# Optimization experiments

Measured on AMD Instinct MI355X. Metric: run time of the kernel, lower is better.

## Reference

```python
import jax, jax.numpy as jnp
import numpy as np

B, P, NP, D, DS, M, K = 2, 4000, 4096, 64, 64, 512, 8
NX, NY = 432, 496
HW = NY * NX


def _per_batch(points, pillars, pillars_scale, idx, W):
    # points: [NP, D], pillars: [P, D], pillars_scale: [P, DS], idx: [P] in [0, HW)
    # --- get_score: top-k point attention per pillar ---
    score = jax.nn.softmax(points @ pillars.T, axis=0)                # [NP, P], softmax over points
    top_idx = jax.lax.top_k(jax.lax.stop_gradient(score).T, K)[1]     # [P, K]
    pts_pos = points[top_idx]                                         # [P, K, D]
    agg = jax.nn.softmax(jnp.einsum('pd,pkd->pk', pillars, pts_pos), axis=1)
    pos_point = jnp.einsum('pk,pkd->pd', jax.lax.stop_gradient(agg), pts_pos)  # [P, D]
    # --- memory unit: top-k memory-item attention per pillar ---
    att = jax.nn.softmax(pillars @ W.T, axis=1)                       # [P, M]
    midx = jax.lax.top_k(jax.lax.stop_gradient(att), K)[1]            # [P, K]
    mem_pos = W[midx]                                                 # [P, K, D]
    magg = jax.nn.softmax(jnp.einsum('pd,pkd->pk', pillars, mem_pos), axis=1)
    pos_mem = jnp.einsum('pk,pkd->pd', magg, mem_pos)                 # [P, D]
    # --- scatter into dense BEV grids ---
    sp_point = jnp.zeros((2 * D, HW), pillars.dtype).at[:, idx].set(
        jnp.concatenate([pillars, pos_point], axis=1).T)
    sp = jnp.zeros((2 * D, HW), pillars.dtype).at[:, idx].set(
        jnp.concatenate([jax.lax.stop_gradient(pillars), pos_mem], axis=1).T)
    sp_scale = jnp.zeros((DS, HW), pillars_scale.dtype).at[:, idx].set(pillars_scale.T)
    return sp, sp_point, sp_scale, pos_point, pos_mem


def setup_inputs() -> dict:
    key = jax.random.key(0)
    k1, k2, k3, k4, k5 = jax.random.split(key, 5)
    return {
        'pillar_features': jax.random.normal(k1, (B, P, D), jnp.float32),
        'pillar_scale_features': jax.random.normal(k2, (B, P, DS), jnp.float32),
        'point_features': jax.random.normal(k3, (B, NP, D), jnp.float32),
        'memory_weight': jax.random.normal(k4, (M, D), jnp.float32),
        'indices': jax.random.randint(k5, (B, P), 0, HW, jnp.int32),
    }


def reference(pillar_features, pillar_scale_features, point_features, memory_weight, indices):
    sp, sp_point, sp_scale, pos_point, pos_mem = jax.vmap(
        _per_batch, in_axes=(0, 0, 0, 0, None))(
        point_features, pillar_features, pillar_scale_features, indices, memory_weight)
    spatial_features = sp.reshape(B, 2 * D, NY, NX)
    spatial_features_point = sp_point.reshape(B, 2 * D, NY, NX)
    spatial_scale_features = sp_scale.reshape(B, DS, NY, NX)
    point_positive_features = pos_point.reshape(B * P, D)
    memory_positive_features = pos_mem.reshape(B * P, D)
    return (spatial_features, spatial_features_point, spatial_scale_features,
            point_positive_features, memory_positive_features)
```

## Files before the change

kernel.cpp:

```cpp
#include <hip/hip_runtime.h>

#define B_     2
#define P_TOT  4000
#define NP_TOT 4096
#define D_     64
#define M_     512
#define HW_TOT 214272
#define J4     53568

#define O0 0UL
#define O1 54853632UL
#define O2 109707264UL
#define O3 137134080UL
#define O4 137646080UL

typedef __attribute__((ext_vector_type(8))) short bb8;
typedef __attribute__((ext_vector_type(4))) float f32x4;

__device__ __forceinline__ void insert8(float sc, int n, float s[8], int ix[8]) {
  float cs = sc; int ci = n;
#pragma unroll
  for (int i = 0; i < 8; ++i) {
    bool gt = cs > s[i];
    float ts = s[i]; int ti = ix[i];
    s[i]  = gt ? cs : ts;  ix[i] = gt ? ci : ti;
    cs    = gt ? ts : cs;  ci    = gt ? ti : ci;
  }
}

__device__ __forceinline__ void split_bf16(float x, short& h, short& l) {
  unsigned fb = __float_as_uint(x);
  unsigned hb = fb & 0xFFFF0000u;
  float lof = x - __uint_as_float(hb);
  h = (short)(hb >> 16);
  l = (short)(__float_as_uint(lof) >> 16);
}

__global__ __launch_bounds__(256) void prep(
    const float* __restrict__ points, short* __restrict__ hi, short* __restrict__ lo,
    const int* __restrict__ indices, int* __restrict__ owner,
    const float* __restrict__ W, short* __restrict__ whi, short* __restrict__ wlo)
{
  if (blockIdx.x < 512) {
    int t = blockIdx.x * 256 + threadIdx.x;
    float4 v = ((const float4*)points)[t];
    float x[4] = {v.x, v.y, v.z, v.w};
    short h[4], l[4];
#pragma unroll
    for (int j = 0; j < 4; ++j) split_bf16(x[j], h[j], l[j]);
    ((short4*)hi)[t] = make_short4(h[0], h[1], h[2], h[3]);
    ((short4*)lo)[t] = make_short4(l[0], l[1], l[2], l[3]);
  } else if (blockIdx.x < 544) {
    int t = (blockIdx.x - 512) * 256 + threadIdx.x;
    if (t >= B_ * P_TOT) return;
    int b = (t >= P_TOT) ? 1 : 0;
    int p = t - b * P_TOT;
    atomicMax(&owner[b * HW_TOT + indices[t]], p);
  } else {
    int t = (blockIdx.x - 544) * 256 + threadIdx.x;
    float4 v = ((const float4*)W)[t];
    float x[4] = {v.x, v.y, v.z, v.w};
    short h[4], l[4];
#pragma unroll
    for (int j = 0; j < 4; ++j) split_bf16(x[j], h[j], l[j]);
    ((short4*)whi)[t] = make_short4(h[0], h[1], h[2], h[3]);
    ((short4*)wlo)[t] = make_short4(l[0], l[1], l[2], l[3]);
  }
}

__global__ __launch_bounds__(256) void topk_mfma(
    const float* __restrict__ pillars,
    const short* __restrict__ phi, const short* __restrict__ plo,
    const short* __restrict__ whi, const short* __restrict__ wlo,
    float* __restrict__ ws_pts_sc, int* __restrict__ ws_pts_ix,
    float* __restrict__ ws_mem_sc, int* __restrict__ ws_mem_ix)
{
  const int tid = threadIdx.x;
  const int pt = blockIdx.x, chy = blockIdx.y, b = blockIdx.z;
  const bool is_mem = chy >= 8;
  const int ch = is_mem ? (chy - 8) : chy;
  const int lane = tid & 63, wv = tid >> 6;
  const int sub = lane & 15, quad = lane >> 4;

  int prow = pt * 64 + wv * 16 + sub;
  if (prow >= P_TOT) prow = P_TOT - 1;
  const float* ap = pillars + ((size_t)(b * P_TOT) + prow) * D_;
  bb8 Ah0, Ah1, Al0, Al1;
  {
    const float4* a4 = (const float4*)(ap + quad * 8);
    const float4* b4 = (const float4*)(ap + 32 + quad * 8);
    float4 t0 = a4[0], t1 = a4[1], t2 = b4[0], t3 = b4[1];
    float av[16] = {t0.x, t0.y, t0.z, t0.w, t1.x, t1.y, t1.z, t1.w,
                    t2.x, t2.y, t2.z, t2.w, t3.x, t3.y, t3.z, t3.w};
#pragma unroll
    for (int j = 0; j < 8; ++j) {
      short h, l;
      split_bf16(av[j], h, l);     Ah0[j] = h; Al0[j] = l;
      split_bf16(av[8 + j], h, l); Ah1[j] = h; Al1[j] = l;
    }
  }

  float sv[4][8]; int iv[4][8];
#pragma unroll
  for (int r = 0; r < 4; ++r)
#pragma unroll
    for (int k = 0; k < 8; ++k) { sv[r][k] = -1e30f; iv[r][k] = 0; }

  const short* bh;
  const short* bl;
  int iters, ngb;
  if (is_mem) {
    bh = whi + (size_t)(ch * 64) * D_;
    bl = wlo + (size_t)(ch * 64) * D_;
    iters = 4;  ngb = ch * 64;
  } else {
    const size_t bofs = ((size_t)(b * NP_TOT) + ch * 512) * D_;
    bh = phi + bofs;  bl = plo + bofs;
    iters = 32; ngb = ch * 512;
  }

#pragma unroll 2
  for (int it = 0; it < iters; ++it) {
    const int nr = it * 16 + sub;
    const short* rh = bh + nr * D_;
    const short* rl = bl + nr * D_;
    bb8 Bh0 = *(const bb8*)(rh + quad * 8);
    bb8 Bh1 = *(const bb8*)(rh + 32 + quad * 8);
    bb8 Bl0 = *(const bb8*)(rl + quad * 8);
    bb8 Bl1 = *(const bb8*)(rl + 32 + quad * 8);
    f32x4 acc = {0.f, 0.f, 0.f, 0.f};
    if (is_mem) {
      acc = __builtin_amdgcn_mfma_f32_16x16x32_bf16(Al0, Bl0, acc, 0, 0, 0);
      acc = __builtin_amdgcn_mfma_f32_16x16x32_bf16(Al1, Bl1, acc, 0, 0, 0);
    }
    acc = __builtin_amdgcn_mfma_f32_16x16x32_bf16(Al0, Bh0, acc, 0, 0, 0);
    acc = __builtin_amdgcn_mfma_f32_16x16x32_bf16(Al1, Bh1, acc, 0, 0, 0);
    acc = __builtin_amdgcn_mfma_f32_16x16x32_bf16(Ah0, Bl0, acc, 0, 0, 0);
    acc = __builtin_amdgcn_mfma_f32_16x16x32_bf16(Ah1, Bl1, acc, 0, 0, 0);
    acc = __builtin_amdgcn_mfma_f32_16x16x32_bf16(Ah0, Bh0, acc, 0, 0, 0);
    acc = __builtin_amdgcn_mfma_f32_16x16x32_bf16(Ah1, Bh1, acc, 0, 0, 0);
    const int ng = ngb + nr;
#pragma unroll
    for (int r = 0; r < 4; ++r) {
      float sc = acc[r];
      if (sc > sv[r][7]) insert8(sc, ng, sv[r], iv[r]);
    }
  }

  float* osc = is_mem ? ws_mem_sc : ws_pts_sc;
  int*   oix = is_mem ? ws_mem_ix : ws_pts_ix;

  const int pbase = pt * 64 + wv * 16 + quad * 4;
#pragma unroll
  for (int r = 0; r < 4; ++r) {
    const int pg = pbase + r;
    float out_s = 0.f; int out_i = 0;
#pragma unroll
    for (int k = 0; k < 8; ++k) {
      unsigned fb = __float_as_uint(sv[r][0]);
      unsigned mk = (fb & 0x80000000u) ? ~fb : (fb | 0x80000000u);
      unsigned key = (mk & 0xFFFFFFF0u) | (unsigned)sub;
#pragma unroll
      for (int off = 1; off < 16; off <<= 1) {
        unsigned ok = (unsigned)__shfl_xor((int)key, off);
        key = key > ok ? key : ok;
      }
      const int wsub = (int)(key & 15u);
      const int wlane = (lane & 48) | wsub;
      float wsc = __shfl(sv[r][0], wlane);
      int   wix = __shfl(iv[r][0], wlane);
      if (sub == wsub) {
#pragma unroll
        for (int i2 = 0; i2 < 7; ++i2) { sv[r][i2] = sv[r][i2 + 1]; iv[r][i2] = iv[r][i2 + 1]; }
        sv[r][7] = -1e30f;
      }
      if (sub == k) { out_s = wsc; out_i = wix; }
    }
    if (sub < 8 && pg < P_TOT) {
      const size_t base = ((size_t)(b * P_TOT) + pg) * 64 + ch * 8 + sub;
      osc[base] = out_s; oix[base] = out_i;
    }
  }
}

__global__ __launch_bounds__(256) void finalize2(
    const float* __restrict__ points, const float* __restrict__ W,
    const float* __restrict__ ws_sc_p, const int* __restrict__ ws_ix_p,
    const float* __restrict__ ws_sc_m, const int* __restrict__ ws_ix_m,
    float* __restrict__ out_p, float* __restrict__ out_m)
{
  const int tid = threadIdx.x;
  const int lane = tid & 63, wv = tid >> 6;
  const int gp = blockIdx.x * 4 + wv;
  const int b = (gp >= P_TOT) ? 1 : 0;
  const size_t cb = (size_t)gp * 64;
  const bool mem = (blockIdx.y == 1);

  const float* ws_sc = mem ? ws_sc_m : ws_sc_p;
  const int*   ws_ix = mem ? ws_ix_m : ws_ix_p;
  const float* sb    = mem ? W : (points + (size_t)b * (NP_TOT * D_));
  float*       outp  = mem ? out_m : out_p;

  float ss = ws_sc[cb + lane];
  const int myix = ws_ix[cb + lane];

  float wsc[8]; int wix[8];
#pragma unroll
  for (int k = 0; k < 8; ++k) {
    float cv = ss; int cl = lane;
#pragma unroll
    for (int off = 32; off >= 1; off >>= 1) {
      float ov = __shfl_xor(cv, off);
      int   ol = __shfl_xor(cl, off);
      if (ov > cv || (ov == cv && ol < cl)) { cv = ov; cl = ol; }
    }
    wsc[k] = cv;
    wix[k] = __shfl(myix, cl);
    if (lane == cl) ss = -1e30f;
  }

  const float m = wsc[0];
  float e[8], Z = 0.f;
#pragma unroll
  for (int k = 0; k < 8; ++k) { e[k] = expf(wsc[k] - m); Z += e[k]; }
  const float inv = 1.0f / Z;

  float acc = 0.f;
#pragma unroll
  for (int k = 0; k < 8; ++k)
    acc = fmaf(e[k] * inv, sb[(size_t)wix[k] * 64 + lane], acc);
  outp[cb + lane] = acc;
}

__global__ __launch_bounds__(256) void scatter5(
    const float* __restrict__ pillars, const float* __restrict__ scale,
    const float* __restrict__ pos_point, const float* __restrict__ pos_mem,
    const int* __restrict__ owner, float* __restrict__ out)
{
  const int j4 = blockIdx.x * 256 + threadIdx.x;
  if (j4 >= J4) return;
  const int cbch = blockIdx.y * 16;
  const int b = blockIdx.z;

  const int4 own = ((const int4*)owner)[(size_t)b * J4 + j4];
  const bool act = (own.x & own.y & own.z & own.w) >= 0;

  const size_t bo = (size_t)b * (P_TOT * D_);
  const float* sp = pillars   + bo;
  const float* sm = pos_mem   + bo;
  const float* sq = pos_point + bo;
  const float* ss = scale     + bo;

  const size_t r0 = (size_t)(own.x < 0 ? 0 : own.x) * 64 + cbch;
  const size_t r1 = (size_t)(own.y < 0 ? 0 : own.y) * 64 + cbch;
  const size_t r2 = (size_t)(own.z < 0 ? 0 : own.z) * 64 + cbch;
  const size_t r3 = (size_t)(own.w < 0 ? 0 : own.w) * 64 + cbch;

  f32x4* o4 = (f32x4*)out;
  const f32x4 zf = {0.f, 0.f, 0.f, 0.f};

#pragma unroll
  for (int q = 0; q < 4; ++q) {
    const int ch = cbch + q * 4;

    {
      f32x4 A0 = zf, A1 = zf, A2 = zf, A3 = zf;
      if (act) {
        A0 = own.x < 0 ? zf : *(const f32x4*)(sp + r0 + q * 4);
        A1 = own.y < 0 ? zf : *(const f32x4*)(sp + r1 + q * 4);
        A2 = own.z < 0 ? zf : *(const f32x4*)(sp + r2 + q * 4);
        A3 = own.w < 0 ? zf : *(const f32x4*)(sp + r3 + q * 4);
      }
#pragma unroll
      for (int dc = 0; dc < 4; ++dc) {
        f32x4 v = {A0[dc], A1[dc], A2[dc], A3[dc]};
        __builtin_nontemporal_store(v, o4 + (size_t)(b * 128 + ch + dc) * J4 + j4);
        __builtin_nontemporal_store(v, o4 + 13713408UL + (size_t)(b * 128 + ch + dc) * J4 + j4);
      }
    }
    {
      f32x4 A0 = zf, A1 = zf, A2 = zf, A3 = zf;
      if (act) {
        A0 = own.x < 0 ? zf : *(const f32x4*)(sm + r0 + q * 4);
        A1 = own.y < 0 ? zf : *(const f32x4*)(sm + r1 + q * 4);
        A2 = own.z < 0 ? zf : *(const f32x4*)(sm + r2 + q * 4);
        A3 = own.w < 0 ? zf : *(const f32x4*)(sm + r3 + q * 4);
      }
#pragma unroll
      for (int dc = 0; dc < 4; ++dc) {
        f32x4 v = {A0[dc], A1[dc], A2[dc], A3[dc]};
        __builtin_nontemporal_store(v, o4 + (size_t)(b * 128 + 64 + ch + dc) * J4 + j4);
      }
    }
    {
      f32x4 A0 = zf, A1 = zf, A2 = zf, A3 = zf;
      if (act) {
        A0 = own.x < 0 ? zf : *(const f32x4*)(sq + r0 + q * 4);
        A1 = own.y < 0 ? zf : *(const f32x4*)(sq + r1 + q * 4);
        A2 = own.z < 0 ? zf : *(const f32x4*)(sq + r2 + q * 4);
        A3 = own.w < 0 ? zf : *(const f32x4*)(sq + r3 + q * 4);
      }
#pragma unroll
      for (int dc = 0; dc < 4; ++dc) {
        f32x4 v = {A0[dc], A1[dc], A2[dc], A3[dc]};
        __builtin_nontemporal_store(v, o4 + 13713408UL + (size_t)(b * 128 + 64 + ch + dc) * J4 + j4);
      }
    }
    {
      f32x4 A0 = zf, A1 = zf, A2 = zf, A3 = zf;
      if (act) {
        A0 = own.x < 0 ? zf : *(const f32x4*)(ss + r0 + q * 4);
        A1 = own.y < 0 ? zf : *(const f32x4*)(ss + r1 + q * 4);
        A2 = own.z < 0 ? zf : *(const f32x4*)(ss + r2 + q * 4);
        A3 = own.w < 0 ? zf : *(const f32x4*)(ss + r3 + q * 4);
      }
#pragma unroll
      for (int dc = 0; dc < 4; ++dc) {
        f32x4 v = {A0[dc], A1[dc], A2[dc], A3[dc]};
        __builtin_nontemporal_store(v, o4 + 27426816UL + (size_t)(b * 64 + ch + dc) * J4 + j4);
      }
    }
  }
}

extern "C" void kernel_launch(void* const* d_in, const int* in_sizes, int n_in,
                              void* d_out, int out_size, void* d_ws, size_t ws_size,
                              hipStream_t stream) {
  const float* pillars = (const float*)d_in[0];
  const float* scale   = (const float*)d_in[1];
  const float* points  = (const float*)d_in[2];
  const float* W       = (const float*)d_in[3];
  const int*   indices = (const int*)d_in[4];
  float* out = (float*)d_out;

  float* ws_pts_sc = (float*)d_ws;
  int*   ws_pts_ix = (int*)d_ws + 512000;
  float* ws_mem_sc = (float*)d_ws + 1024000;
  int*   ws_mem_ix = (int*)d_ws + 1536000;
  int*   owner     = (int*)d_ws + 2048000;
  short* phi       = (short*)((int*)d_ws + 2480000);
  short* plo       = (short*)((int*)d_ws + 2760000);
  short* whi       = (short*)((int*)d_ws + 3030000);
  short* wlo       = (short*)((int*)d_ws + 3050000);

  (void)hipMemsetAsync(owner, 0xFF, (size_t)B_ * HW_TOT * sizeof(int), stream);

  prep<<<576, 256, 0, stream>>>(points, phi, plo, indices, owner, W, whi, wlo);

  topk_mfma<<<dim3(63, 16, 2), 256, 0, stream>>>(
      pillars, phi, plo, whi, wlo, ws_pts_sc, ws_pts_ix, ws_mem_sc, ws_mem_ix);

  finalize2<<<dim3(2000, 2), 256, 0, stream>>>(
      points, W, ws_pts_sc, ws_pts_ix, ws_mem_sc, ws_mem_ix, out + O3, out + O4);

  scatter5<<<dim3(210, 4, 2), 256, 0, stream>>>(
      pillars, scale, out + O3, out + O4, owner, out);
}
```

Measured before the change: 660.5 us.

## Fuse static-input scatter into top-k kernel to overlap stores with compute

The dense-grid writes that depend only on inputs (pillar copies into both spatial outputs and the scale grid) move out of the final scatter kernel. They become extra blocks interleaved within the top-k MFMA launch. This lets the memory-bound stores run concurrently with the compute-bound top-k blocks, and leaves only the result-dependent channels for the last scatter. The cost is a larger, heterogeneous grid in which scatter blocks may compete for bandwidth and CU slots with top-k blocks.

```diff
diff --git a/kernel.cpp b/kernel.cpp
--- a/kernel.cpp
+++ b/kernel.cpp
@@ -68,15 +68,79 @@
   }
 }
 
-__global__ __launch_bounds__(256) void topk_mfma(
-    const float* __restrict__ pillars,
+__global__ __launch_bounds__(256) void topk_sstat(
+    const float* __restrict__ pillars, const float* __restrict__ scale,
     const short* __restrict__ phi, const short* __restrict__ plo,
     const short* __restrict__ whi, const short* __restrict__ wlo,
+    const int* __restrict__ owner,
     float* __restrict__ ws_pts_sc, int* __restrict__ ws_pts_ix,
-    float* __restrict__ ws_mem_sc, int* __restrict__ ws_mem_ix)
+    float* __restrict__ ws_mem_sc, int* __restrict__ ws_mem_ix,
+    float* __restrict__ out)
 {
+  const int g = blockIdx.x / 11, r11 = blockIdx.x % 11;
+  const int b = blockIdx.z;
+
+  if (r11 >= 6) {
+    const int six = g * 5 + (r11 - 6);
+    const int jblk = six % 210, ych = six / 210;
+    const int j4 = jblk * 256 + threadIdx.x;
+    if (j4 >= J4) return;
+    const int cbch = ych * 16;
+
+    const int4 own = ((const int4*)owner)[(size_t)b * J4 + j4];
+    const bool act = (own.x & own.y & own.z & own.w) >= 0;
+
+    const size_t bo = (size_t)b * (P_TOT * D_);
+    const float* sp = pillars + bo;
+    const float* ssc = scale  + bo;
+
+    const size_t r0 = (size_t)(own.x < 0 ? 0 : own.x) * 64 + cbch;
+    const size_t r1 = (size_t)(own.y < 0 ? 0 : own.y) * 64 + cbch;
+    const size_t r2 = (size_t)(own.z < 0 ? 0 : own.z) * 64 + cbch;
+    const size_t r3 = (size_t)(own.w < 0 ? 0 : own.w) * 64 + cbch;
+
+    f32x4* o4 = (f32x4*)out;
+    const f32x4 zf = {0.f, 0.f, 0.f, 0.f};
+
+#pragma unroll
+    for (int q = 0; q < 4; ++q) {
+      const int ch = cbch + q * 4;
+      {
+        f32x4 A0 = zf, A1 = zf, A2 = zf, A3 = zf;
+        if (act) {
+          A0 = own.x < 0 ? zf : *(const f32x4*)(sp + r0 + q * 4);
+          A1 = own.y < 0 ? zf : *(const f32x4*)(sp + r1 + q * 4);
+          A2 = own.z < 0 ? zf : *(const f32x4*)(sp + r2 + q * 4);
+          A3 = own.w < 0 ? zf : *(const f32x4*)(sp + r3 + q * 4);
+        }
+#pragma unroll
+        for (int dc = 0; dc < 4; ++dc) {
+          f32x4 v = {A0[dc], A1[dc], A2[dc], A3[dc]};
+          __builtin_nontemporal_store(v, o4 + (size_t)(b * 128 + ch + dc) * J4 + j4);
+          __builtin_nontemporal_store(v, o4 + 13713408UL + (size_t)(b * 128 + ch + dc) * J4 + j4);
+        }
+      }
+      {
+        f32x4 A0 = zf, A1 = zf, A2 = zf, A3 = zf;
+        if (act) {
+          A0 = own.x < 0 ? zf : *(const f32x4*)(ssc + r0 + q * 4);
+          A1 = own.y < 0 ? zf : *(const f32x4*)(ssc + r1 + q * 4);
+          A2 = own.z < 0 ? zf : *(const f32x4*)(ssc + r2 + q * 4);
+          A3 = own.w < 0 ? zf : *(const f32x4*)(ssc + r3 + q * 4);
+        }
+#pragma unroll
+        for (int dc = 0; dc < 4; ++dc) {
+          f32x4 v = {A0[dc], A1[dc], A2[dc], A3[dc]};
+          __builtin_nontemporal_store(v, o4 + 27426816UL + (size_t)(b * 64 + ch + dc) * J4 + j4);
+        }
+      }
+    }
+    return;
+  }
+
+  const int tix = g * 6 + r11;
+  const int pt = tix % 63, chy = tix / 63;
   const int tid = threadIdx.x;
-  const int pt = blockIdx.x, chy = blockIdx.y, b = blockIdx.z;
   const bool is_mem = chy >= 8;
   const int ch = is_mem ? (chy - 8) : chy;
   const int lane = tid & 63, wv = tid >> 6;
@@ -232,8 +296,7 @@
   outp[cb + lane] = acc;
 }
 
-__global__ __launch_bounds__(256) void scatter5(
-    const float* __restrict__ pillars, const float* __restrict__ scale,
+__global__ __launch_bounds__(256) void scatter_dyn(
     const float* __restrict__ pos_point, const float* __restrict__ pos_mem,
     const int* __restrict__ owner, float* __restrict__ out)
 {
@@ -246,10 +309,8 @@
   const bool act = (own.x & own.y & own.z & own.w) >= 0;
 
   const size_t bo = (size_t)b * (P_TOT * D_);
-  const float* sp = pillars   + bo;
   const float* sm = pos_mem   + bo;
   const float* sq = pos_point + bo;
-  const float* ss = scale     + bo;
 
   const size_t r0 = (size_t)(own.x < 0 ? 0 : own.x) * 64 + cbch;
   const size_t r1 = (size_t)(own.y < 0 ? 0 : own.y) * 64 + cbch;
@@ -262,22 +323,6 @@
 #pragma unroll
   for (int q = 0; q < 4; ++q) {
     const int ch = cbch + q * 4;
-
-    {
-      f32x4 A0 = zf, A1 = zf, A2 = zf, A3 = zf;
-      if (act) {
-        A0 = own.x < 0 ? zf : *(const f32x4*)(sp + r0 + q * 4);
-        A1 = own.y < 0 ? zf : *(const f32x4*)(sp + r1 + q * 4);
-        A2 = own.z < 0 ? zf : *(const f32x4*)(sp + r2 + q * 4);
-        A3 = own.w < 0 ? zf : *(const f32x4*)(sp + r3 + q * 4);
-      }
-#pragma unroll
-      for (int dc = 0; dc < 4; ++dc) {
-        f32x4 v = {A0[dc], A1[dc], A2[dc], A3[dc]};
-        __builtin_nontemporal_store(v, o4 + (size_t)(b * 128 + ch + dc) * J4 + j4);
-        __builtin_nontemporal_store(v, o4 + 13713408UL + (size_t)(b * 128 + ch + dc) * J4 + j4);
-      }
-    }
     {
       f32x4 A0 = zf, A1 = zf, A2 = zf, A3 = zf;
       if (act) {
@@ -304,20 +349,6 @@
       for (int dc = 0; dc < 4; ++dc) {
         f32x4 v = {A0[dc], A1[dc], A2[dc], A3[dc]};
         __builtin_nontemporal_store(v, o4 + 13713408UL + (size_t)(b * 128 + 64 + ch + dc) * J4 + j4);
-      }
-    }
-    {
-      f32x4 A0 = zf, A1 = zf, A2 = zf, A3 = zf;
-      if (act) {
-        A0 = own.x < 0 ? zf : *(const f32x4*)(ss + r0 + q * 4);
-        A1 = own.y < 0 ? zf : *(const f32x4*)(ss + r1 + q * 4);
-        A2 = own.z < 0 ? zf : *(const f32x4*)(ss + r2 + q * 4);
-        A3 = own.w < 0 ? zf : *(const f32x4*)(ss + r3 + q * 4);
-      }
-#pragma unroll
-      for (int dc = 0; dc < 4; ++dc) {
-        f32x4 v = {A0[dc], A1[dc], A2[dc], A3[dc]};
-        __builtin_nontemporal_store(v, o4 + 27426816UL + (size_t)(b * 64 + ch + dc) * J4 + j4);
       }
     }
   }
@@ -347,12 +378,13 @@
 
   prep<<<576, 256, 0, stream>>>(points, phi, plo, indices, owner, W, whi, wlo);
 
-  topk_mfma<<<dim3(63, 16, 2), 256, 0, stream>>>(
-      pillars, phi, plo, whi, wlo, ws_pts_sc, ws_pts_ix, ws_mem_sc, ws_mem_ix);
+  topk_sstat<<<dim3(1848, 1, 2), 256, 0, stream>>>(
+      pillars, scale, phi, plo, whi, wlo, owner,
+      ws_pts_sc, ws_pts_ix, ws_mem_sc, ws_mem_ix, out);
 
   finalize2<<<dim3(2000, 2), 256, 0, stream>>>(
       points, W, ws_pts_sc, ws_pts_ix, ws_mem_sc, ws_mem_ix, out + O3, out + O4);
 
-  scatter5<<<dim3(210, 4, 2), 256, 0, stream>>>(
-      pillars, scale, out + O3, out + O4, owner, out);
-}
+  scatter_dyn<<<dim3(210, 4, 2), 256, 0, stream>>>(
+      out + O3, out + O4, owner, out);
+}
```

After: 634.5 us (median of 2 runs). -3.9%, faster.
